# Optimization experiments

Measured on AMD Instinct MI355X. Metric: run time of the kernel, lower is better.

The kernel has to match this reference:

```python
import jax, jax.numpy as jnp
import numpy as np

#   forward = type-A masked 5x5 conv: [n,C,H,W] -> [n,K,C,H,W] logits
#   sample_fn = categorical over the K (value) dimension
N, C, H, W, K, KS = 64, 3, 12, 12, 128, 5


def _mask(ks):
    # Type-A raster mask: only strictly-preceding pixels visible (center excluded)
    m = np.ones((ks, ks), np.float32)
    c = ks // 2
    m[c, c:] = 0.0
    m[c + 1:, :] = 0.0
    return jnp.asarray(m)


def setup_inputs() -> dict:
    key = jax.random.key(0)
    kw, _ = jax.random.split(key)
    # _get_conditioned_on: unconditional sample -> ones * -1 (all pixels to be sampled)
    conditioned_on = -jnp.ones((N, C, H, W), jnp.float32)
    Wc = jax.random.normal(kw, (K * C, C, KS, KS), jnp.float32) * 0.05
    b = jnp.zeros((K * C,), jnp.float32)
    return {"conditioned_on": conditioned_on, "Wc": Wc, "b": b}


def _forward(x, Wc, b):
    # Masked conv -> logits [n, K, C, H, W]
    y = jax.lax.conv_general_dilated(
        x, Wc * _mask(KS), (1, 1), "SAME",
        dimension_numbers=("NCHW", "OIHW", "NCHW"))
    y = y + b[None, :, None, None]
    return y.reshape(x.shape[0], K, C, H, W)


def reference(conditioned_on, Wc, b):
    n = conditioned_on.shape[0]
    hw = H * W
    base_key = jax.random.key(42)

    def body(i, img):
        # Full forward recompute every pixel step (faithful to torch sample loop)
        logits = _forward(img, Wc, b).reshape(n, K, C, hw)
        li = jax.lax.dynamic_index_in_dim(logits, i, axis=3, keepdims=False)  # [n,K,C]
        samp = jax.random.categorical(jax.random.fold_in(base_key, i), li, axis=1)
        samp = samp.astype(img.dtype)  # [n,C]
        flat = img.reshape(n, C, hw)
        cur = jax.lax.dynamic_index_in_dim(flat, i, axis=2, keepdims=False)  # [n,C]
        new = jnp.where(cur < 0, samp, cur)  # only fill unobserved (<0) pixels
        flat = flat.at[:, :, i].set(new)
        return flat.reshape(n, C, H, W)

    # row-major (row, col) double loop == raster-order flat index loop
    return jax.lax.fori_loop(0, hw, body, conditioned_on)
```

## Files before the change

kernel.cpp:

```cpp
#include <hip/hip_runtime.h>
#include <stdint.h>

#define NB 64
#define CC 3
#define HH 12
#define WW 12
#define HW 144
#define KC 384
#define TINYF 1.17549435e-38f
#ifndef PARTITIONABLE
#define PARTITIONABLE 1
#endif

__device__ __forceinline__ void tf2x32(uint32_t k0, uint32_t k1,
                                       uint32_t& x0, uint32_t& x1) {
  const uint32_t ks2 = k0 ^ k1 ^ 0x1BD11BDAu;
  x0 += k0; x1 += k1;
#define RND(r) { x0 += x1; x1 = (x1 << (r)) | (x1 >> (32 - (r))); x1 ^= x0; }
  RND(13) RND(15) RND(26) RND(6)   x0 += k1;  x1 += ks2 + 1u;
  RND(17) RND(29) RND(16) RND(24)  x0 += ks2; x1 += k0 + 2u;
  RND(13) RND(15) RND(26) RND(6)   x0 += k0;  x1 += k1 + 3u;
  RND(17) RND(29) RND(16) RND(24)  x0 += k1;  x1 += ks2 + 4u;
  RND(13) RND(15) RND(26) RND(6)   x0 += ks2; x1 += k0 + 5u;
#undef RND
}

__device__ __forceinline__ uint32_t rbits(uint32_t k0, uint32_t k1, uint32_t e) {
#if PARTITIONABLE == 1
  uint32_t x0 = 0u, x1 = e;
  tf2x32(k0, k1, x0, x1);
  return x0 ^ x1;
#else
  const uint32_t half = (uint32_t)(NB * KC / 2);
  const bool lo = e < half;
  uint32_t x0 = lo ? e : e - half;
  uint32_t x1 = lo ? e + half : e;
  tf2x32(k0, k1, x0, x1);
  return lo ? x0 : x1;
#endif
}

__device__ __forceinline__ float gumbel32(uint32_t k0, uint32_t k1, uint32_t e) {
  const uint32_t bits = rbits(k0, k1, e);
  const float f = __uint_as_float((bits >> 9) | 0x3f800000u) - 1.0f;
  const float u = fmaxf(TINYF, f + TINYF);
  return (float)(-log(-log((double)u)));
}

__global__ __launch_bounds__(256) void gumbel_pre(float* __restrict__ gws) {
  const uint32_t tid = blockIdx.x * 256u + threadIdx.x;
  const uint32_t t  = tid % KC;
  const uint32_t c  = t >> 7, k = t & 127u;
  const uint32_t ni = tid / KC;
  const uint32_t i  = ni % HW;
  const uint32_t n  = ni / HW;
  uint32_t a = 0u, b = i;
  tf2x32(0u, 42u, a, b);
  gws[tid] = gumbel32(a, b, n * KC + k * 3u + c);
}

template<int CTRL>
__device__ __forceinline__ float dpp_max_step(float v) {
  const int o = __builtin_amdgcn_update_dpp(0xFF800000, __float_as_int(v),
                                            CTRL, 0xF, 0xF, false);
  return fmaxf(v, __int_as_float(o));
}
__device__ __forceinline__ float wave_max_bcast(float v) {
  v = dpp_max_step<0x111>(v);
  v = dpp_max_step<0x112>(v);
  v = dpp_max_step<0x114>(v);
  v = dpp_max_step<0x118>(v);
  v = dpp_max_step<0x142>(v);
  v = dpp_max_step<0x143>(v);
  return __int_as_float(__builtin_amdgcn_readlane(__float_as_int(v), 63));
}

template<bool PRE>
__global__ __launch_bounds__(192, 1) void ar_sample(
    const float* __restrict__ cond,
    const float* __restrict__ Wc,
    const float* __restrict__ bias,
    const float* __restrict__ gws,
    float* __restrict__ out)
{
  __shared__ float4   xp4[HH + 2][WW + 4];
  __shared__ float4   outb[HW];
  __shared__ float    cndl[CC * HW];
  __shared__ uint32_t k0s[HW], k1s[HW];

  const int n    = blockIdx.x;
  const int t    = threadIdx.x;
  const int lane = t & 63;
  const int cw   = t >> 6;
  float* outf = (float*)outb;

  double wdA[CC][12], wdB[CC][12];
#pragma unroll
  for (int ci = 0; ci < CC; ++ci)
#pragma unroll
    for (int tap = 0; tap < 12; ++tap) {
      const int kh = tap < 10 ? tap / 5 : 2;
      const int kw = tap < 10 ? tap % 5 : tap - 10;
      wdA[ci][tap] = (double)Wc[(lane * 3 + cw) * 75 + ci * 25 + kh * 5 + kw];
      wdB[ci][tap] = (double)Wc[((lane + 64) * 3 + cw) * 75 + ci * 25 + kh * 5 + kw];
    }
  const float bA = bias[lane * 3 + cw];
  const float bB = bias[(lane + 64) * 3 + cw];

  for (int idx = t; idx < (HH + 2) * (WW + 4); idx += 192)
    ((float4*)xp4)[idx] = make_float4(0.f, 0.f, 0.f, 0.f);
  for (int idx = t; idx < CC * HW; idx += 192)
    cndl[idx] = cond[n * CC * HW + idx];
  if (!PRE && t < HW) {
    uint32_t a = 0u, b = (uint32_t)t;
    tf2x32(0u, 42u, a, b);
    k0s[t] = a; k1s[t] = b;
  }
  __syncthreads();

  float gA[WW], gB[WW], nAr[WW], nBr[WW], cr[WW];
  if (PRE) {
#pragma unroll
    for (int w = 0; w < WW; ++w) {
      nAr[w] = gws[(n * HW + w) * KC + cw * 128 + lane];
      nBr[w] = gws[(n * HW + w) * KC + cw * 128 + 64 + lane];
    }
  } else {
#pragma unroll
    for (int w = 0; w < WW; ++w) {
      nAr[w] = gumbel32(k0s[w], k1s[w], n * KC + lane * 3 + cw);
      nBr[w] = gumbel32(k0s[w], k1s[w], n * KC + (lane + 64) * 3 + cw);
    }
  }

  double partA = 0.0, partB = 0.0;
  float sA0 = 0.f, sA1 = 0.f, sA2 = 0.f;
  float sB0 = 0.f, sB1 = 0.f, sB2 = 0.f;

  for (int h = 0; h < HH; ++h) {
#pragma unroll
    for (int w = 0; w < WW; ++w) { gA[w] = nAr[w]; gB[w] = nBr[w]; }
#pragma unroll
    for (int w = 0; w < WW; ++w) cr[w] = cndl[cw * HW + h * WW + w];
    if (h + 1 < HH) {
      if (PRE) {
#pragma unroll
        for (int w = 0; w < WW; ++w) {
          const int i2 = (h + 1) * WW + w;
          nAr[w] = gws[(n * HW + i2) * KC + cw * 128 + lane];
          nBr[w] = gws[(n * HW + i2) * KC + cw * 128 + 64 + lane];
        }
      } else {
#pragma unroll
        for (int w = 0; w < WW; ++w) {
          const int i2 = (h + 1) * WW + w;
          nAr[w] = gumbel32(k0s[i2], k1s[i2], n * KC + lane * 3 + cw);
          nBr[w] = gumbel32(k0s[i2], k1s[i2], n * KC + (lane + 64) * 3 + cw);
        }
      }
    }

#pragma unroll
    for (int w = 0; w < WW; ++w) {
      const int i = h * WW + w;

      const int h2 = (w == WW - 1) ? h + 1 : h;
      const int w2 = (w == WW - 1) ? 0 : w + 1;
      float4 px[10];
#pragma unroll
      for (int tap = 0; tap < 10; ++tap)
        px[tap] = xp4[h2 + tap / 5][w2 + tap % 5];

      double tA = partA, tB = partB;
      if (w >= 1) {
        tA += ((double)sA0 * wdA[0][11] + (double)sA1 * wdA[1][11]) + (double)sA2 * wdA[2][11];
        tB += ((double)sA0 * wdB[0][11] + (double)sA1 * wdB[1][11]) + (double)sA2 * wdB[2][11];
      }
      if (w >= 2) {
        tA += ((double)sB0 * wdA[0][10] + (double)sB1 * wdA[1][10]) + (double)sB2 * wdA[2][10];
        tB += ((double)sB0 * wdB[0][10] + (double)sB1 * wdB[1][10]) + (double)sB2 * wdB[2][10];
      }
      const float vA = ((float)tA + bA) + gA[w];
      const float vB = ((float)tB + bB) + gB[w];

      const float vm   = fmaxf(vA, vB);
      const float smax = wave_max_bcast(vm);
      const unsigned long long aM = __ballot(vA == smax);
      const unsigned long long bM = __ballot(vB == smax);
      const int kwin = aM ? (int)__builtin_ctzll(aM)
                          : (int)__builtin_ctzll(bM) + 64;

      const float cv   = cr[w];
      const float sNew = (cv < 0.f) ? (float)kwin : cv;
      if (lane == 0) outf[i * 4 + cw] = sNew;

      asm volatile("s_waitcnt lgkmcnt(0)" ::: "memory");
      __builtin_amdgcn_s_barrier();
      __builtin_amdgcn_sched_barrier(0);

      const float4 ex = outb[i];
      sB0 = sA0; sB1 = sA1; sB2 = sA2;
      sA0 = ex.x; sA1 = ex.y; sA2 = ex.z;
      if (t == 0) xp4[h + 2][w + 2] = make_float4(sA0, sA1, sA2, 0.f);

      double pA0 = 0, pA1 = 0, pB0 = 0, pB1 = 0;
#pragma unroll
      for (int tap = 0; tap < 10; ++tap) {
        const float4 v = px[tap];
        if (tap & 1) {
          pA1 = fma((double)v.x, wdA[0][tap], pA1);
          pA1 = fma((double)v.y, wdA[1][tap], pA1);
          pA1 = fma((double)v.z, wdA[2][tap], pA1);
          pB1 = fma((double)v.x, wdB[0][tap], pB1);
          pB1 = fma((double)v.y, wdB[1][tap], pB1);
          pB1 = fma((double)v.z, wdB[2][tap], pB1);
        } else {
          pA0 = fma((double)v.x, wdA[0][tap], pA0);
          pA0 = fma((double)v.y, wdA[1][tap], pA0);
          pA0 = fma((double)v.z, wdA[2][tap], pA0);
          pB0 = fma((double)v.x, wdB[0][tap], pB0);
          pB0 = fma((double)v.y, wdB[1][tap], pB0);
          pB0 = fma((double)v.z, wdB[2][tap], pB0);
        }
      }
      partA = pA0 + pA1; partB = pB0 + pB1;
    }
  }

  __syncthreads();
  for (int idx = t; idx < CC * HW; idx += 192) {
    const int c = idx / HW, i = idx - c * HW;
    out[n * CC * HW + idx] = outf[i * 4 + c];
  }
}

extern "C" void kernel_launch(void* const* d_in, const int* in_sizes, int n_in,
                              void* d_out, int out_size, void* d_ws, size_t ws_size,
                              hipStream_t stream) {
  const float* cond = (const float*)d_in[0];
  const float* Wc   = (const float*)d_in[1];
  const float* b    = (const float*)d_in[2];
  float* out = (float*)d_out;
  const size_t need = (size_t)NB * HW * KC * sizeof(float);
  if (ws_size >= need) {
    float* gws = (float*)d_ws;
    hipLaunchKernelGGL(gumbel_pre, dim3((NB * HW * KC) / 256), dim3(256), 0,
                       stream, gws);
    hipLaunchKernelGGL((ar_sample<true>), dim3(NB), dim3(192), 0, stream,
                       cond, Wc, b, gws, out);
  } else {
    hipLaunchKernelGGL((ar_sample<false>), dim3(NB), dim3(192), 0, stream,
                       cond, Wc, b, (const float*)nullptr, out);
  }
}
```

Measured before the change: 172.3 us.

## Split sampler into producer/consumer waves with pipelined partial conv sums

Doubles the block to 384 threads. Three waves now run the serial argmax/sample chain, and three producer waves compute the 10-tap partial convolution two pixels ahead, passing results through a 4-slot shared-memory ring. The goal is to take the 60 fp64 FMAs per pixel off the critical serial path and lower register pressure in the sampling waves, which also get raised priority. This adds shared-memory traffic and relies on the per-pixel barrier being shared by both wave groups, so any mismatch in barrier counts would deadlock or race.

```diff
diff --git a/kernel.cpp b/kernel.cpp
--- a/kernel.cpp
+++ b/kernel.cpp
@@ -76,7 +76,7 @@
 }
 
 template<bool PRE>
-__global__ __launch_bounds__(192, 1) void ar_sample(
+__global__ __launch_bounds__(384, 1) void ar_sample(
     const float* __restrict__ cond,
     const float* __restrict__ Wc,
     const float* __restrict__ bias,
@@ -86,31 +86,20 @@
   __shared__ float4   xp4[HH + 2][WW + 4];
   __shared__ float4   outb[HW];
   __shared__ float    cndl[CC * HW];
+  __shared__ double   pd[4][KC];
   __shared__ uint32_t k0s[HW], k1s[HW];
 
   const int n    = blockIdx.x;
   const int t    = threadIdx.x;
   const int lane = t & 63;
-  const int cw   = t >> 6;
   float* outf = (float*)outb;
 
-  double wdA[CC][12], wdB[CC][12];
-#pragma unroll
-  for (int ci = 0; ci < CC; ++ci)
-#pragma unroll
-    for (int tap = 0; tap < 12; ++tap) {
-      const int kh = tap < 10 ? tap / 5 : 2;
-      const int kw = tap < 10 ? tap % 5 : tap - 10;
-      wdA[ci][tap] = (double)Wc[(lane * 3 + cw) * 75 + ci * 25 + kh * 5 + kw];
-      wdB[ci][tap] = (double)Wc[((lane + 64) * 3 + cw) * 75 + ci * 25 + kh * 5 + kw];
-    }
-  const float bA = bias[lane * 3 + cw];
-  const float bB = bias[(lane + 64) * 3 + cw];
-
-  for (int idx = t; idx < (HH + 2) * (WW + 4); idx += 192)
+  for (int idx = t; idx < (HH + 2) * (WW + 4); idx += 384)
     ((float4*)xp4)[idx] = make_float4(0.f, 0.f, 0.f, 0.f);
-  for (int idx = t; idx < CC * HW; idx += 192)
+  for (int idx = t; idx < CC * HW; idx += 384)
     cndl[idx] = cond[n * CC * HW + idx];
+#pragma unroll
+  for (int s = 0; s < 4; ++s) pd[s][t] = 0.0;
   if (!PRE && t < HW) {
     uint32_t a = 0u, b = (uint32_t)t;
     tf2x32(0u, 42u, a, b);
@@ -118,117 +107,155 @@
   }
   __syncthreads();
 
-  float gA[WW], gB[WW], nAr[WW], nBr[WW], cr[WW];
-  if (PRE) {
-#pragma unroll
-    for (int w = 0; w < WW; ++w) {
-      nAr[w] = gws[(n * HW + w) * KC + cw * 128 + lane];
-      nBr[w] = gws[(n * HW + w) * KC + cw * 128 + 64 + lane];
+  if (t < 192) {
+    const int cw = t >> 6;
+    double wA10[3], wA11[3], wB10[3], wB11[3];
+#pragma unroll
+    for (int ci = 0; ci < 3; ++ci) {
+      wA10[ci] = (double)Wc[(lane * 3 + cw) * 75 + ci * 25 + 10];
+      wA11[ci] = (double)Wc[(lane * 3 + cw) * 75 + ci * 25 + 11];
+      wB10[ci] = (double)Wc[((lane + 64) * 3 + cw) * 75 + ci * 25 + 10];
+      wB11[ci] = (double)Wc[((lane + 64) * 3 + cw) * 75 + ci * 25 + 11];
+    }
+    const float bA = bias[lane * 3 + cw];
+    const float bB = bias[(lane + 64) * 3 + cw];
+
+    float gA[WW], gB[WW], nAr[WW], nBr[WW], cr[WW];
+    if (PRE) {
+#pragma unroll
+      for (int w = 0; w < WW; ++w) {
+        nAr[w] = gws[(n * HW + w) * KC + cw * 128 + lane];
+        nBr[w] = gws[(n * HW + w) * KC + cw * 128 + 64 + lane];
+      }
+    } else {
+#pragma unroll
+      for (int w = 0; w < WW; ++w) {
+        nAr[w] = gumbel32(k0s[w], k1s[w], n * KC + lane * 3 + cw);
+        nBr[w] = gumbel32(k0s[w], k1s[w], n * KC + (lane + 64) * 3 + cw);
+      }
+    }
+
+    double pdAc = 0.0, pdBc = 0.0;
+    double pdAn = 0.0, pdBn = 0.0;
+    float sA0 = 0.f, sA1 = 0.f, sA2 = 0.f;
+    float sB0 = 0.f, sB1 = 0.f, sB2 = 0.f;
+    __builtin_amdgcn_s_setprio(1);
+
+    for (int h = 0; h < HH; ++h) {
+#pragma unroll
+      for (int w = 0; w < WW; ++w) { gA[w] = nAr[w]; gB[w] = nBr[w]; }
+#pragma unroll
+      for (int w = 0; w < WW; ++w) cr[w] = cndl[cw * HW + h * WW + w];
+      if (h + 1 < HH) {
+        if (PRE) {
+#pragma unroll
+          for (int w = 0; w < WW; ++w) {
+            const int i2 = (h + 1) * WW + w;
+            nAr[w] = gws[(n * HW + i2) * KC + cw * 128 + lane];
+            nBr[w] = gws[(n * HW + i2) * KC + cw * 128 + 64 + lane];
+          }
+        } else {
+#pragma unroll
+          for (int w = 0; w < WW; ++w) {
+            const int i2 = (h + 1) * WW + w;
+            nAr[w] = gumbel32(k0s[i2], k1s[i2], n * KC + lane * 3 + cw);
+            nBr[w] = gumbel32(k0s[i2], k1s[i2], n * KC + (lane + 64) * 3 + cw);
+          }
+        }
+      }
+
+#pragma unroll
+      for (int w = 0; w < WW; ++w) {
+        const int i = h * WW + w;
+
+        double tA = pdAc, tB = pdBc;
+        if (w >= 1) {
+          tA += ((double)sA0 * wA11[0] + (double)sA1 * wA11[1]) + (double)sA2 * wA11[2];
+          tB += ((double)sA0 * wB11[0] + (double)sA1 * wB11[1]) + (double)sA2 * wB11[2];
+        }
+        if (w >= 2) {
+          tA += ((double)sB0 * wA10[0] + (double)sB1 * wA10[1]) + (double)sB2 * wA10[2];
+          tB += ((double)sB0 * wB10[0] + (double)sB1 * wB10[1]) + (double)sB2 * wB10[2];
+        }
+        const float vA = ((float)tA + bA) + gA[w];
+        const float vB = ((float)tB + bB) + gB[w];
+
+        const float vm   = fmaxf(vA, vB);
+        const float smax = wave_max_bcast(vm);
+        const unsigned long long aM = __ballot(vA == smax);
+        const unsigned long long bM = __ballot(vB == smax);
+        const int kwin = aM ? (int)__builtin_ctzll(aM)
+                            : (int)__builtin_ctzll(bM) + 64;
+
+        const float cv   = cr[w];
+        const float sNew = (cv < 0.f) ? (float)kwin : cv;
+        if (lane == 0) outf[i * 4 + cw] = sNew;
+
+        asm volatile("s_waitcnt lgkmcnt(0)" ::: "memory");
+        __builtin_amdgcn_s_barrier();
+        __builtin_amdgcn_sched_barrier(0);
+
+        const float4 ex = outb[i];
+        pdAc = pdAn; pdBc = pdBn;
+        if (i + 2 < HW) {
+          pdAn = pd[(i + 2) & 3][cw * 128 + lane];
+          pdBn = pd[(i + 2) & 3][cw * 128 + 64 + lane];
+        }
+        sB0 = sA0; sB1 = sA1; sB2 = sA2;
+        sA0 = ex.x; sA1 = ex.y; sA2 = ex.z;
+        if (t == 0) xp4[h + 2][w + 2] = make_float4(ex.x, ex.y, ex.z, 0.f);
+      }
     }
   } else {
-#pragma unroll
-    for (int w = 0; w < WW; ++w) {
-      nAr[w] = gumbel32(k0s[w], k1s[w], n * KC + lane * 3 + cw);
-      nBr[w] = gumbel32(k0s[w], k1s[w], n * KC + (lane + 64) * 3 + cw);
-    }
-  }
-
-  double partA = 0.0, partB = 0.0;
-  float sA0 = 0.f, sA1 = 0.f, sA2 = 0.f;
-  float sB0 = 0.f, sB1 = 0.f, sB2 = 0.f;
-
-  for (int h = 0; h < HH; ++h) {
-#pragma unroll
-    for (int w = 0; w < WW; ++w) { gA[w] = nAr[w]; gB[w] = nBr[w]; }
-#pragma unroll
-    for (int w = 0; w < WW; ++w) cr[w] = cndl[cw * HW + h * WW + w];
-    if (h + 1 < HH) {
-      if (PRE) {
-#pragma unroll
-        for (int w = 0; w < WW; ++w) {
-          const int i2 = (h + 1) * WW + w;
-          nAr[w] = gws[(n * HW + i2) * KC + cw * 128 + lane];
-          nBr[w] = gws[(n * HW + i2) * KC + cw * 128 + 64 + lane];
-        }
-      } else {
-#pragma unroll
-        for (int w = 0; w < WW; ++w) {
-          const int i2 = (h + 1) * WW + w;
-          nAr[w] = gumbel32(k0s[i2], k1s[i2], n * KC + lane * 3 + cw);
-          nBr[w] = gumbel32(k0s[i2], k1s[i2], n * KC + (lane + 64) * 3 + cw);
-        }
-      }
-    }
-
-#pragma unroll
-    for (int w = 0; w < WW; ++w) {
-      const int i = h * WW + w;
-
-      const int h2 = (w == WW - 1) ? h + 1 : h;
-      const int w2 = (w == WW - 1) ? 0 : w + 1;
-      float4 px[10];
-#pragma unroll
-      for (int tap = 0; tap < 10; ++tap)
-        px[tap] = xp4[h2 + tap / 5][w2 + tap % 5];
-
-      double tA = partA, tB = partB;
-      if (w >= 1) {
-        tA += ((double)sA0 * wdA[0][11] + (double)sA1 * wdA[1][11]) + (double)sA2 * wdA[2][11];
-        tB += ((double)sA0 * wdB[0][11] + (double)sA1 * wdB[1][11]) + (double)sA2 * wdB[2][11];
-      }
-      if (w >= 2) {
-        tA += ((double)sB0 * wdA[0][10] + (double)sB1 * wdA[1][10]) + (double)sB2 * wdA[2][10];
-        tB += ((double)sB0 * wdB[0][10] + (double)sB1 * wdB[1][10]) + (double)sB2 * wdB[2][10];
-      }
-      const float vA = ((float)tA + bA) + gA[w];
-      const float vB = ((float)tB + bB) + gB[w];
-
-      const float vm   = fmaxf(vA, vB);
-      const float smax = wave_max_bcast(vm);
-      const unsigned long long aM = __ballot(vA == smax);
-      const unsigned long long bM = __ballot(vB == smax);
-      const int kwin = aM ? (int)__builtin_ctzll(aM)
-                          : (int)__builtin_ctzll(bM) + 64;
-
-      const float cv   = cr[w];
-      const float sNew = (cv < 0.f) ? (float)kwin : cv;
-      if (lane == 0) outf[i * 4 + cw] = sNew;
-
+    const int cw = (t >> 6) - 3;
+    double wS[3][10], wT[3][10];
+#pragma unroll
+    for (int ci = 0; ci < 3; ++ci)
+#pragma unroll
+      for (int tap = 0; tap < 10; ++tap) {
+        wS[ci][tap] = (double)Wc[(lane * 3 + cw) * 75 + ci * 25 + tap];
+        wT[ci][tap] = (double)Wc[((lane + 64) * 3 + cw) * 75 + ci * 25 + tap];
+      }
+
+    for (int i = 0; i < HW; ++i) {
+      const int j = i + 2;
+      if (j < HW) {
+        const int hj = j / WW, wj = j - hj * WW;
+        float4 px[10];
+#pragma unroll
+        for (int tap = 0; tap < 10; ++tap)
+          px[tap] = xp4[hj + tap / 5][wj + tap % 5];
+        double pA0 = 0, pA1 = 0, pB0 = 0, pB1 = 0;
+#pragma unroll
+        for (int tap = 0; tap < 10; ++tap) {
+          const float4 v = px[tap];
+          if (tap & 1) {
+            pA1 = fma((double)v.x, wS[0][tap], pA1);
+            pA1 = fma((double)v.y, wS[1][tap], pA1);
+            pA1 = fma((double)v.z, wS[2][tap], pA1);
+            pB1 = fma((double)v.x, wT[0][tap], pB1);
+            pB1 = fma((double)v.y, wT[1][tap], pB1);
+            pB1 = fma((double)v.z, wT[2][tap], pB1);
+          } else {
+            pA0 = fma((double)v.x, wS[0][tap], pA0);
+            pA0 = fma((double)v.y, wS[1][tap], pA0);
+            pA0 = fma((double)v.z, wS[2][tap], pA0);
+            pB0 = fma((double)v.x, wT[0][tap], pB0);
+            pB0 = fma((double)v.y, wT[1][tap], pB0);
+            pB0 = fma((double)v.z, wT[2][tap], pB0);
+          }
+        }
+        pd[j & 3][cw * 128 + lane]      = pA0 + pA1;
+        pd[j & 3][cw * 128 + 64 + lane] = pB0 + pB1;
+      }
       asm volatile("s_waitcnt lgkmcnt(0)" ::: "memory");
       __builtin_amdgcn_s_barrier();
       __builtin_amdgcn_sched_barrier(0);
-
-      const float4 ex = outb[i];
-      sB0 = sA0; sB1 = sA1; sB2 = sA2;
-      sA0 = ex.x; sA1 = ex.y; sA2 = ex.z;
-      if (t == 0) xp4[h + 2][w + 2] = make_float4(sA0, sA1, sA2, 0.f);
-
-      double pA0 = 0, pA1 = 0, pB0 = 0, pB1 = 0;
-#pragma unroll
-      for (int tap = 0; tap < 10; ++tap) {
-        const float4 v = px[tap];
-        if (tap & 1) {
-          pA1 = fma((double)v.x, wdA[0][tap], pA1);
-          pA1 = fma((double)v.y, wdA[1][tap], pA1);
-          pA1 = fma((double)v.z, wdA[2][tap], pA1);
-          pB1 = fma((double)v.x, wdB[0][tap], pB1);
-          pB1 = fma((double)v.y, wdB[1][tap], pB1);
-          pB1 = fma((double)v.z, wdB[2][tap], pB1);
-        } else {
-          pA0 = fma((double)v.x, wdA[0][tap], pA0);
-          pA0 = fma((double)v.y, wdA[1][tap], pA0);
-          pA0 = fma((double)v.z, wdA[2][tap], pA0);
-          pB0 = fma((double)v.x, wdB[0][tap], pB0);
-          pB0 = fma((double)v.y, wdB[1][tap], pB0);
-          pB0 = fma((double)v.z, wdB[2][tap], pB0);
-        }
-      }
-      partA = pA0 + pA1; partB = pB0 + pB1;
     }
   }
 
   __syncthreads();
-  for (int idx = t; idx < CC * HW; idx += 192) {
+  for (int idx = t; idx < CC * HW; idx += 384) {
     const int c = idx / HW, i = idx - c * HW;
     out[n * CC * HW + idx] = outf[i * 4 + c];
   }
@@ -246,10 +273,10 @@
     float* gws = (float*)d_ws;
     hipLaunchKernelGGL(gumbel_pre, dim3((NB * HW * KC) / 256), dim3(256), 0,
                        stream, gws);
-    hipLaunchKernelGGL((ar_sample<true>), dim3(NB), dim3(192), 0, stream,
+    hipLaunchKernelGGL((ar_sample<true>), dim3(NB), dim3(384), 0, stream,
                        cond, Wc, b, gws, out);
   } else {
-    hipLaunchKernelGGL((ar_sample<false>), dim3(NB), dim3(192), 0, stream,
+    hipLaunchKernelGGL((ar_sample<false>), dim3(NB), dim3(384), 0, stream,
                        cond, Wc, b, (const float*)nullptr, out);
   }
 }
```

New measurement: 161.1 us. 1.07x faster.

## Split sampling into a critical-path wave and shadow waves computing conv partials ahead

Applied to the files above, without the earlier changes.

The block grows from 3 to 7 waves. One wave handles the serial argmax chain for all three channels, using only the two most recent same-row taps. The other six waves compute the 10-tap masked-conv partial sums a few pixels ahead and pass them through a 4-slot shared ring buffer. This takes the bulk of the per-pixel FP64 convolution off the serial critical path and drops the cross-wave channel exchange through shared memory. The cost is three serial wave reductions per pixel in a single wave and a barrier shared across 7 waves.

```diff
diff --git a/kernel.cpp b/kernel.cpp
--- a/kernel.cpp
+++ b/kernel.cpp
@@ -75,8 +75,14 @@
   return __int_as_float(__builtin_amdgcn_readlane(__float_as_int(v), 63));
 }
 
+#define REGION_BARRIER() do {                               \
+    asm volatile("s_waitcnt lgkmcnt(0)" ::: "memory");      \
+    __builtin_amdgcn_s_barrier();                           \
+    __builtin_amdgcn_sched_barrier(0);                      \
+  } while (0)
+
 template<bool PRE>
-__global__ __launch_bounds__(192, 1) void ar_sample(
+__global__ __launch_bounds__(448, 1) void ar_sample(
     const float* __restrict__ cond,
     const float* __restrict__ Wc,
     const float* __restrict__ bias,
@@ -84,33 +90,18 @@
     float* __restrict__ out)
 {
   __shared__ float4   xp4[HH + 2][WW + 4];
-  __shared__ float4   outb[HW];
   __shared__ float    cndl[CC * HW];
+  __shared__ double   pd[4][KC];
   __shared__ uint32_t k0s[HW], k1s[HW];
 
-  const int n    = blockIdx.x;
-  const int t    = threadIdx.x;
-  const int lane = t & 63;
-  const int cw   = t >> 6;
-  float* outf = (float*)outb;
-
-  double wdA[CC][12], wdB[CC][12];
-#pragma unroll
-  for (int ci = 0; ci < CC; ++ci)
-#pragma unroll
-    for (int tap = 0; tap < 12; ++tap) {
-      const int kh = tap < 10 ? tap / 5 : 2;
-      const int kw = tap < 10 ? tap % 5 : tap - 10;
-      wdA[ci][tap] = (double)Wc[(lane * 3 + cw) * 75 + ci * 25 + kh * 5 + kw];
-      wdB[ci][tap] = (double)Wc[((lane + 64) * 3 + cw) * 75 + ci * 25 + kh * 5 + kw];
-    }
-  const float bA = bias[lane * 3 + cw];
-  const float bB = bias[(lane + 64) * 3 + cw];
-
-  for (int idx = t; idx < (HH + 2) * (WW + 4); idx += 192)
+  const int n = blockIdx.x, t = threadIdx.x, lane = t & 63;
+
+  for (int idx = t; idx < (HH + 2) * (WW + 4); idx += 448)
     ((float4*)xp4)[idx] = make_float4(0.f, 0.f, 0.f, 0.f);
-  for (int idx = t; idx < CC * HW; idx += 192)
+  for (int idx = t; idx < CC * HW; idx += 448)
     cndl[idx] = cond[n * CC * HW + idx];
+  for (int idx = t; idx < 4 * KC; idx += 448)
+    ((double*)pd)[idx] = 0.0;
   if (!PRE && t < HW) {
     uint32_t a = 0u, b = (uint32_t)t;
     tf2x32(0u, 42u, a, b);
@@ -118,119 +109,153 @@
   }
   __syncthreads();
 
-  float gA[WW], gB[WW], nAr[WW], nBr[WW], cr[WW];
-  if (PRE) {
-#pragma unroll
-    for (int w = 0; w < WW; ++w) {
-      nAr[w] = gws[(n * HW + w) * KC + cw * 128 + lane];
-      nBr[w] = gws[(n * HW + w) * KC + cw * 128 + 64 + lane];
+  if (t < 64) {
+    double w11[6][3], w10[6][3];
+    float  bs[6];
+#pragma unroll
+    for (int c = 0; c < 3; ++c)
+#pragma unroll
+      for (int j = 0; j < 2; ++j) {
+        const int o = c * 2 + j, k = lane + j * 64;
+#pragma unroll
+        for (int ci = 0; ci < 3; ++ci) {
+          w11[o][ci] = (double)Wc[(k * 3 + c) * 75 + ci * 25 + 11];
+          w10[o][ci] = (double)Wc[(k * 3 + c) * 75 + ci * 25 + 10];
+        }
+        bs[o] = bias[k * 3 + c];
+      }
+    float gum[6][4];
+    if (PRE) {
+#pragma unroll
+      for (int p = 0; p < 3; ++p)
+#pragma unroll
+        for (int c = 0; c < 3; ++c)
+#pragma unroll
+          for (int j = 0; j < 2; ++j)
+            gum[c * 2 + j][p] = gws[(n * HW + p) * KC + c * 128 + lane + j * 64];
+    }
+    float cnd_cur[3], cnd_nxt[3];
+#pragma unroll
+    for (int c = 0; c < 3; ++c) cnd_cur[c] = cndl[c * HW + 0];
+    double pdc[6] = {0, 0, 0, 0, 0, 0}, pdn[6];
+    double e11[6], e10[6];
+    float sA0 = 0.f, sA1 = 0.f, sA2 = 0.f;
+    __builtin_amdgcn_s_setprio(1);
+
+    for (int h = 0; h < HH; ++h) {
+#pragma unroll
+      for (int w = 0; w < WW; ++w) {
+        const int i = h * WW + w;
+#pragma unroll
+        for (int c = 0; c < 3; ++c)
+#pragma unroll
+          for (int j = 0; j < 2; ++j)
+            pdn[c * 2 + j] = pd[(w + 1) & 3][c * 128 + lane + j * 64];
+        {
+          const int i1 = (i + 1 < HW) ? i + 1 : HW - 1;
+#pragma unroll
+          for (int c = 0; c < 3; ++c) cnd_nxt[c] = cndl[c * HW + i1];
+        }
+        if (PRE) {
+          const int i3 = (i + 3 < HW) ? i + 3 : HW - 1;
+#pragma unroll
+          for (int c = 0; c < 3; ++c)
+#pragma unroll
+            for (int j = 0; j < 2; ++j)
+              gum[c * 2 + j][(w + 3) & 3] =
+                  gws[(n * HW + i3) * KC + c * 128 + lane + j * 64];
+        }
+        float v[6];
+#pragma unroll
+        for (int o = 0; o < 6; ++o) {
+          double tA = pdc[o];
+          if (w >= 1) tA += e11[o];
+          if (w >= 2) tA += e10[o];
+          float g;
+          if (PRE) g = gum[o][w & 3];
+          else {
+            const int c = o >> 1, k = lane + (o & 1) * 64;
+            g = gumbel32(k0s[i], k1s[i], n * KC + k * 3 + c);
+          }
+          v[o] = ((float)tA + bs[o]) + g;
+        }
+        float sN[3];
+#pragma unroll
+        for (int c = 0; c < 3; ++c) {
+          const float vm   = fmaxf(v[c * 2], v[c * 2 + 1]);
+          const float smax = wave_max_bcast(vm);
+          const unsigned long long aM = __ballot(v[c * 2] == smax);
+          const unsigned long long bM = __ballot(v[c * 2 + 1] == smax);
+          const int kwin = aM ? (int)__builtin_ctzll(aM)
+                              : (int)__builtin_ctzll(bM) + 64;
+          sN[c] = (cnd_cur[c] < 0.f) ? (float)kwin : cnd_cur[c];
+        }
+        if (lane == 0) xp4[h + 2][w + 2] = make_float4(sN[0], sN[1], sN[2], 0.f);
+#pragma unroll
+        for (int o = 0; o < 6; ++o) {
+          e11[o] = ((double)sN[0] * w11[o][0] + (double)sN[1] * w11[o][1])
+                 +  (double)sN[2] * w11[o][2];
+          e10[o] = ((double)sA0 * w10[o][0] + (double)sA1 * w10[o][1])
+                 +  (double)sA2 * w10[o][2];
+        }
+        sA0 = sN[0]; sA1 = sN[1]; sA2 = sN[2];
+        REGION_BARRIER();
+#pragma unroll
+        for (int o = 0; o < 6; ++o) pdc[o] = pdn[o];
+#pragma unroll
+        for (int c = 0; c < 3; ++c) cnd_cur[c] = cnd_nxt[c];
+      }
     }
   } else {
-#pragma unroll
-    for (int w = 0; w < WW; ++w) {
-      nAr[w] = gumbel32(k0s[w], k1s[w], n * KC + lane * 3 + cw);
-      nBr[w] = gumbel32(k0s[w], k1s[w], n * KC + (lane + 64) * 3 + cw);
-    }
-  }
-
-  double partA = 0.0, partB = 0.0;
-  float sA0 = 0.f, sA1 = 0.f, sA2 = 0.f;
-  float sB0 = 0.f, sB1 = 0.f, sB2 = 0.f;
-
-  for (int h = 0; h < HH; ++h) {
-#pragma unroll
-    for (int w = 0; w < WW; ++w) { gA[w] = nAr[w]; gB[w] = nBr[w]; }
-#pragma unroll
-    for (int w = 0; w < WW; ++w) cr[w] = cndl[cw * HW + h * WW + w];
-    if (h + 1 < HH) {
-      if (PRE) {
-#pragma unroll
-        for (int w = 0; w < WW; ++w) {
-          const int i2 = (h + 1) * WW + w;
-          nAr[w] = gws[(n * HW + i2) * KC + cw * 128 + lane];
-          nBr[w] = gws[(n * HW + i2) * KC + cw * 128 + 64 + lane];
-        }
-      } else {
-#pragma unroll
-        for (int w = 0; w < WW; ++w) {
-          const int i2 = (h + 1) * WW + w;
-          nAr[w] = gumbel32(k0s[i2], k1s[i2], n * KC + lane * 3 + cw);
-          nBr[w] = gumbel32(k0s[i2], k1s[i2], n * KC + (lane + 64) * 3 + cw);
-        }
-      }
-    }
-
-#pragma unroll
-    for (int w = 0; w < WW; ++w) {
-      const int i = h * WW + w;
-
-      const int h2 = (w == WW - 1) ? h + 1 : h;
-      const int w2 = (w == WW - 1) ? 0 : w + 1;
-      float4 px[10];
+    const int o = t - 64;
+    const int c = o >> 7, k = o & 127;
+    double wsd[3][10];
+#pragma unroll
+    for (int ci = 0; ci < 3; ++ci)
 #pragma unroll
       for (int tap = 0; tap < 10; ++tap)
-        px[tap] = xp4[h2 + tap / 5][w2 + tap % 5];
-
-      double tA = partA, tB = partB;
-      if (w >= 1) {
-        tA += ((double)sA0 * wdA[0][11] + (double)sA1 * wdA[1][11]) + (double)sA2 * wdA[2][11];
-        tB += ((double)sA0 * wdB[0][11] + (double)sA1 * wdB[1][11]) + (double)sA2 * wdB[2][11];
-      }
-      if (w >= 2) {
-        tA += ((double)sB0 * wdA[0][10] + (double)sB1 * wdA[1][10]) + (double)sB2 * wdA[2][10];
-        tB += ((double)sB0 * wdB[0][10] + (double)sB1 * wdB[1][10]) + (double)sB2 * wdB[2][10];
-      }
-      const float vA = ((float)tA + bA) + gA[w];
-      const float vB = ((float)tB + bB) + gB[w];
-
-      const float vm   = fmaxf(vA, vB);
-      const float smax = wave_max_bcast(vm);
-      const unsigned long long aM = __ballot(vA == smax);
-      const unsigned long long bM = __ballot(vB == smax);
-      const int kwin = aM ? (int)__builtin_ctzll(aM)
-                          : (int)__builtin_ctzll(bM) + 64;
-
-      const float cv   = cr[w];
-      const float sNew = (cv < 0.f) ? (float)kwin : cv;
-      if (lane == 0) outf[i * 4 + cw] = sNew;
-
-      asm volatile("s_waitcnt lgkmcnt(0)" ::: "memory");
-      __builtin_amdgcn_s_barrier();
-      __builtin_amdgcn_sched_barrier(0);
-
-      const float4 ex = outb[i];
-      sB0 = sA0; sB1 = sA1; sB2 = sA2;
-      sA0 = ex.x; sA1 = ex.y; sA2 = ex.z;
-      if (t == 0) xp4[h + 2][w + 2] = make_float4(sA0, sA1, sA2, 0.f);
-
-      double pA0 = 0, pA1 = 0, pB0 = 0, pB1 = 0;
-#pragma unroll
-      for (int tap = 0; tap < 10; ++tap) {
-        const float4 v = px[tap];
-        if (tap & 1) {
-          pA1 = fma((double)v.x, wdA[0][tap], pA1);
-          pA1 = fma((double)v.y, wdA[1][tap], pA1);
-          pA1 = fma((double)v.z, wdA[2][tap], pA1);
-          pB1 = fma((double)v.x, wdB[0][tap], pB1);
-          pB1 = fma((double)v.y, wdB[1][tap], pB1);
-          pB1 = fma((double)v.z, wdB[2][tap], pB1);
-        } else {
-          pA0 = fma((double)v.x, wdA[0][tap], pA0);
-          pA0 = fma((double)v.y, wdA[1][tap], pA0);
-          pA0 = fma((double)v.z, wdA[2][tap], pA0);
-          pB0 = fma((double)v.x, wdB[0][tap], pB0);
-          pB0 = fma((double)v.y, wdB[1][tap], pB0);
-          pB0 = fma((double)v.z, wdB[2][tap], pB0);
-        }
-      }
-      partA = pA0 + pA1; partB = pB0 + pB1;
-    }
+        wsd[ci][tap] = (double)Wc[(k * 3 + c) * 75 + ci * 25 + tap];
+
+    float4 pxA[10], pxB[10];
+
+#define SHADOW_REGION(r, pxC, pxF) {                                         \
+      const int j2 = ((r) + 3 < HW) ? (r) + 3 : HW - 1;                      \
+      const int hj = j2 / WW, wj = j2 - hj * WW;                             \
+      _Pragma("unroll")                                                      \
+      for (int tap = 0; tap < 10; ++tap)                                     \
+        pxF[tap] = xp4[hj + tap / 5][wj + tap % 5];                          \
+      if ((r) >= 1 && (r) <= HW - 3) {     \
+        double p0 = 0.0, p1 = 0.0;                                           \
+        _Pragma("unroll")                                                    \
+        for (int tap = 0; tap < 10; ++tap) {                                 \
+          const float4 vv = pxC[tap];                                        \
+          if (tap & 1) {                                                     \
+            p1 = fma((double)vv.x, wsd[0][tap], p1);                         \
+            p1 = fma((double)vv.y, wsd[1][tap], p1);                         \
+            p1 = fma((double)vv.z, wsd[2][tap], p1);                         \
+          } else {                                                           \
+            p0 = fma((double)vv.x, wsd[0][tap], p0);                         \
+            p0 = fma((double)vv.y, wsd[1][tap], p0);                         \
+            p0 = fma((double)vv.z, wsd[2][tap], p0);                         \
+          }                                                                  \
+        }                                                                    \
+        pd[((r) + 2) & 3][o] = p0 + p1;          \
+      }                                                                      \
+      REGION_BARRIER();                                                      \
+    }
+
+    for (int r = 0; r < HW; r += 2) {
+      SHADOW_REGION(r,     pxA, pxB)
+      SHADOW_REGION(r + 1, pxB, pxA)
+    }
+#undef SHADOW_REGION
   }
 
   __syncthreads();
-  for (int idx = t; idx < CC * HW; idx += 192) {
+  for (int idx = t; idx < CC * HW; idx += 448) {
     const int c = idx / HW, i = idx - c * HW;
-    out[n * CC * HW + idx] = outf[i * 4 + c];
+    const int h = i / WW, w = i - h * WW;
+    out[n * CC * HW + idx] = ((const float*)&xp4[h + 2][w + 2])[c];
   }
 }
 
@@ -246,10 +271,10 @@
     float* gws = (float*)d_ws;
     hipLaunchKernelGGL(gumbel_pre, dim3((NB * HW * KC) / 256), dim3(256), 0,
                        stream, gws);
-    hipLaunchKernelGGL((ar_sample<true>), dim3(NB), dim3(192), 0, stream,
+    hipLaunchKernelGGL((ar_sample<true>), dim3(NB), dim3(448), 0, stream,
                        cond, Wc, b, gws, out);
   } else {
-    hipLaunchKernelGGL((ar_sample<false>), dim3(NB), dim3(192), 0, stream,
+    hipLaunchKernelGGL((ar_sample<false>), dim3(NB), dim3(448), 0, stream,
                        cond, Wc, b, (const float*)nullptr, out);
   }
 }
```

After: 155.6 us. -9.7%, faster.
